# Kernel optimization log

Measured on AMD Instinct MI355X. Metric: run time of the kernel, lower is better.

## Reference

```python
import jax, jax.numpy as jnp
import numpy as np

N = 1_000_000      # number of samples
C = 100            # number of classes
N_BINS = 20        # adaptive-ECE bins (equal-count)
TEMPERATURE = 1.0


def setup_inputs() -> dict:
    key = jax.random.key(0)
    k1, k2 = jax.random.split(key)
    logits = jax.random.normal(k1, (N, C), dtype=jnp.float32)
    labels = jax.random.randint(k2, (N,), 0, C)
    return {"logits": logits, "labels": labels}


def reference(logits, labels):
    # softmax with temperature, top-1 confidence + prediction
    softmaxes = jax.nn.softmax(logits / TEMPERATURE, axis=1)
    confidences = jnp.max(softmaxes, axis=1)            # [N]
    predictions = jnp.argmax(softmaxes, axis=1)         # [N]
    accuracies = (predictions == labels).astype(confidences.dtype)  # [N]

    # sort by confidence ascending; carry accuracies along
    order = jnp.argsort(confidences)
    conf_sorted = confidences[order]
    acc_sorted = accuracies[order]

    num = logits.shape[0]
    window = num // N_BINS            # samples per adaptive bin
    n_full = num // window            # number of flushed bins (== N_BINS when divisible)
    m = n_full * window

    # equal-count binning == reshape + mean (replaces the per-sample python loop)
    conf_bins = conf_sorted[:m].reshape(n_full, window).mean(axis=1)  # avg conf / bin
    acc_bins = acc_sorted[:m].reshape(n_full, window).mean(axis=1)    # accuracy / bin

    ece = jnp.sum(jnp.abs(conf_bins - acc_bins)) * (window / num)
    return jnp.reshape(ece, (1,)), acc_bins
```

## Files before the change

### kernel.cpp

```cpp
#include <hip/hip_runtime.h>
#include <stdint.h>

typedef uint32_t u32;
typedef uint64_t u64;
typedef uint8_t  u8;

#define KEY_MIN   0x3C000000u
#define SUBSHIFT  10
#define NBUCK     57344
#define NBINS     20
#define NB        19

__device__ __forceinline__ u32 bucket_of(u32 key) {
    if (key < KEY_MIN) return 0u;
    u32 b = (key - KEY_MIN) >> SUBSHIFT;
    return b < (u32)NBUCK ? b : (u32)(NBUCK - 1);
}

__global__ __launch_bounds__(256) void k1_conf100(
        const float* __restrict__ logits, const int* __restrict__ labels,
        u32* __restrict__ keys, u8* __restrict__ accb, u32* __restrict__ hist,
        int N) {
    const int C4 = 25;
    int lane = threadIdx.x & 63;
    int wid  = (blockIdx.x * (blockDim.x >> 6)) + (threadIdx.x >> 6);
    int g    = lane >> 4;
    int sub  = lane & 15;
    int r    = wid * 4 + g;
    if (r >= N) return;

    const float4* row4 = (const float4*)(logits + (size_t)r * 100);
    float4 v0 = row4[sub];
    float4 v1;
    bool has2 = (sub + 16) < C4;
    if (has2) v1 = row4[sub + 16];
    else      v1 = make_float4(-3.4e38f, -3.4e38f, -3.4e38f, -3.4e38f);

    float m = v0.x; int am = 4 * sub;
    if (v0.y > m) { m = v0.y; am = 4 * sub + 1; }
    if (v0.z > m) { m = v0.z; am = 4 * sub + 2; }
    if (v0.w > m) { m = v0.w; am = 4 * sub + 3; }
    int b2 = 64 + 4 * sub;
    if (v1.x > m) { m = v1.x; am = b2; }
    if (v1.y > m) { m = v1.y; am = b2 + 1; }
    if (v1.z > m) { m = v1.z; am = b2 + 2; }
    if (v1.w > m) { m = v1.w; am = b2 + 3; }

    #pragma unroll
    for (int off = 8; off >= 1; off >>= 1) {
        float om = __shfl_xor(m, off);
        int   oa = __shfl_xor(am, off);
        if (om > m || (om == m && oa < am)) { m = om; am = oa; }
    }

    float s = __expf(v0.x - m) + __expf(v0.y - m) + __expf(v0.z - m) + __expf(v0.w - m);
    if (has2) s += __expf(v1.x - m) + __expf(v1.y - m) + __expf(v1.z - m) + __expf(v1.w - m);
    #pragma unroll
    for (int off = 8; off >= 1; off >>= 1) s += __shfl_xor(s, off);

    if (sub == 0) {
        float conf = 1.0f / s;
        u32 key = __float_as_uint(conf);
        keys[r] = key;
        accb[r] = (labels[r] == am) ? (u8)1 : (u8)0;
        atomicAdd(&hist[bucket_of(key)], 1u);
    }
}

__global__ __launch_bounds__(256) void k1_generic(
        const float* __restrict__ logits, const int* __restrict__ labels,
        u32* __restrict__ keys, u8* __restrict__ accb, u32* __restrict__ hist,
        int N, int C) {
    int i = blockIdx.x * blockDim.x + threadIdx.x;
    if (i >= N) return;
    const float* row = logits + (size_t)i * (size_t)C;
    float m = -3.4e38f, s = 0.f;
    int am = 0;
    for (int c = 0; c < C; c++) {
        float v = row[c];
        float nm = fmaxf(m, v); am = (v > m) ? c : am;
        s = s * __expf(m - nm) + __expf(v - nm); m = nm;
    }
    float conf = 1.0f / s;
    u32 key = __float_as_uint(conf);
    keys[i] = key;
    accb[i] = (labels[i] == am) ? (u8)1 : (u8)0;
    atomicAdd(&hist[bucket_of(key)], 1u);
}

__global__ void k2_scan(const u32* __restrict__ hist, u32* __restrict__ meta,
                        u32 W) {
    __shared__ u32 sp[1024];
    int t = threadIdx.x;
    const int PER = NBUCK / 1024;
    u32 s = 0;
    for (int k = 0; k < PER; k++) s += hist[t * PER + k];
    sp[t] = s; __syncthreads();
    for (int d = 1; d < 1024; d <<= 1) {
        u32 v = (t >= d) ? sp[t - d] : 0u;
        __syncthreads();
        sp[t] += v;
        __syncthreads();
    }
    u32 cum = sp[t] - s;
    for (int k = 0; k < PER; k++) {
        u32 c = hist[t * PER + k];
        if (c) {
            for (int j = 0; j < NB; j++) {
                u32 r = (u32)(j + 1) * W;
                if (cum < r && r <= cum + c) {
                    meta[j] = (u32)(t * PER + k);
                    meta[NB + j] = r - cum;
                }
            }
        }
        cum += c;
    }
}

__global__ __launch_bounds__(256) void k3_subhist(
        const u32* __restrict__ keys, const u32* __restrict__ meta,
        u32* __restrict__ subhist, int N) {
    __shared__ u32 sB[NB];
    if (threadIdx.x < NB) sB[threadIdx.x] = meta[threadIdx.x];
    __syncthreads();
    int total4 = N >> 2;
    const uint4* k4 = (const uint4*)keys;
    for (int i = blockIdx.x * blockDim.x + threadIdx.x; i < total4;
         i += gridDim.x * blockDim.x) {
        uint4 kv = k4[i];
        u32 ks[4] = {kv.x, kv.y, kv.z, kv.w};
        #pragma unroll
        for (int e = 0; e < 4; e++) {
            u32 b = bucket_of(ks[e]);
            #pragma unroll
            for (int j = 0; j < NB; j++)
                if (b == sB[j]) atomicAdd(&subhist[j * 1024 + (ks[e] & 1023u)], 1u);
        }
    }
    for (int i = (total4 << 2) + blockIdx.x * blockDim.x + threadIdx.x; i < N;
         i += gridDim.x * blockDim.x) {
        u32 k = keys[i];
        u32 b = bucket_of(k);
        for (int j = 0; j < NB; j++)
            if (b == sB[j]) atomicAdd(&subhist[j * 1024 + (k & 1023u)], 1u);
    }
}

__global__ void k4_resolve(const u32* __restrict__ subhist, u32* __restrict__ meta) {
    int j = blockIdx.x;
    int t = threadIdx.x;
    __shared__ u32 sh[256];
    u32 v[4];
    #pragma unroll
    for (int k = 0; k < 4; k++) v[k] = subhist[j * 1024 + t * 4 + k];
    u32 tsum = v[0] + v[1] + v[2] + v[3];
    sh[t] = tsum; __syncthreads();
    for (int d = 1; d < 256; d <<= 1) {
        u32 x = (t >= d) ? sh[t - d] : 0u;
        __syncthreads(); sh[t] += x; __syncthreads();
    }
    u32 run = sh[t] - tsum;
    u32 off = meta[NB + j];
    u32 bkt = meta[j];
    #pragma unroll
    for (int k = 0; k < 4; k++) {
        if (run < off && off <= run + v[k])
            meta[2 * NB + j] = KEY_MIN + (bkt << SUBSHIFT) + (u32)(t * 4 + k);
        run += v[k];
    }
}

__global__ __launch_bounds__(256) void k7_accum(
        const u32* __restrict__ keys, const u8* __restrict__ accb,
        const u32* __restrict__ meta, u64* __restrict__ confQ,
        u32* __restrict__ accCnt, int N) {
    __shared__ unsigned long long lc[4][NBINS];
    __shared__ u32 la[4][NBINS];
    __shared__ u32 sK[NB];
    int t = threadIdx.x;
    int w = t >> 6;
    if (t < 4 * NBINS) { lc[t / NBINS][t % NBINS] = 0ull; la[t / NBINS][t % NBINS] = 0u; }
    if (t < NB) sK[t] = meta[2 * NB + t];
    __syncthreads();
    int total4 = N >> 2;
    const uint4*  k4 = (const uint4*)keys;
    const uchar4* a4 = (const uchar4*)accb;
    for (int i = blockIdx.x * blockDim.x + t; i < total4; i += gridDim.x * blockDim.x) {
        uint4  kv = k4[i];
        uchar4 av = a4[i];
        u32 ks[4] = {kv.x, kv.y, kv.z, kv.w};
        u32 as[4] = {av.x, av.y, av.z, av.w};
        #pragma unroll
        for (int e = 0; e < 4; e++) {
            int bin = 0;
            #pragma unroll
            for (int j = 0; j < NB; j++) bin += (ks[e] > sK[j]) ? 1 : 0;
            float conf = __uint_as_float(ks[e]);
            u64 q = (u64)(conf * 4294967296.0f);
            atomicAdd(&lc[w][bin], (unsigned long long)q);
            atomicAdd(&la[w][bin], as[e]);
        }
    }
    for (int i = (total4 << 2) + blockIdx.x * blockDim.x + t; i < N;
         i += gridDim.x * blockDim.x) {
        u32 k = keys[i];
        int bin = 0;
        for (int j = 0; j < NB; j++) bin += (k > sK[j]) ? 1 : 0;
        u64 q = (u64)(__uint_as_float(k) * 4294967296.0f);
        atomicAdd(&lc[w][bin], (unsigned long long)q);
        atomicAdd(&la[w][bin], (u32)accb[i]);
    }
    __syncthreads();
    if (t < NBINS) {
        unsigned long long cq = lc[0][t] + lc[1][t] + lc[2][t] + lc[3][t];
        u32 ac = la[0][t] + la[1][t] + la[2][t] + la[3][t];
        if (cq) atomicAdd((unsigned long long*)&confQ[t], cq);
        if (ac) atomicAdd(&accCnt[t], ac);
    }
}

__global__ void k8_final(const u64* __restrict__ confQ, const u32* __restrict__ accCnt,
                         float* __restrict__ out, int W, int N) {
    if (threadIdx.x == 0 && blockIdx.x == 0) {
        double ece = 0.0;
        for (int b = 0; b < NBINS; b++) {
            double cm = (double)confQ[b] * (1.0 / 4294967296.0) / (double)W;
            double am = (double)accCnt[b] / (double)W;
            ece += fabs(cm - am);
            out[1 + b] = (float)am;
        }
        out[0] = (float)(ece * (double)W / (double)N);
    }
}

extern "C" void kernel_launch(void* const* d_in, const int* in_sizes, int n_in,
                              void* d_out, int out_size, void* d_ws, size_t ws_size,
                              hipStream_t stream) {
    const float* logits = (const float*)d_in[0];
    const int*   labels = (const int*)d_in[1];
    int N = in_sizes[1];
    int C = in_sizes[0] / N;
    float* out = (float*)d_out;

    u8* ws = (u8*)d_ws;
    u32* keys = (u32*)ws;
    u8*  accb = ws + (size_t)4 * N;
    size_t aux = ((size_t)5 * N + 255) & ~(size_t)255;
    u64* confQ   = (u64*)(ws + aux);
    u32* accCnt  = (u32*)(ws + aux + 160);
    u32* hist    = (u32*)(ws + aux + 256);
    u32* subhist = (u32*)(ws + aux + 229632);
    u32* meta    = (u32*)(ws + aux + 307456);
    size_t zbytes = 307456 + 228;

    hipMemsetAsync(ws + aux, 0, zbytes, stream);

    u32 W = (u32)(N / NBINS);

    if (C == 100) {
        int blocks1 = (N + 15) / 16;
        k1_conf100<<<blocks1, 256, 0, stream>>>(logits, labels, keys, accb, hist, N);
    } else {
        int blocks1 = (N + 255) / 256;
        k1_generic<<<blocks1, 256, 0, stream>>>(logits, labels, keys, accb, hist, N, C);
    }
    k2_scan   <<<1, 1024, 0, stream>>>(hist, meta, W);
    k3_subhist<<<1024, 256, 0, stream>>>(keys, meta, subhist, N);
    k4_resolve<<<NB, 256, 0, stream>>>(subhist, meta);
    k7_accum  <<<1024, 256, 0, stream>>>(keys, accb, meta, confQ, accCnt, N);
    k8_final  <<<1, 64, 0, stream>>>(confQ, accCnt, out, (int)W, N);
}
```

Baseline: 190.5 us.

## Grid-stride softmax with prefetch, coarser histogram, fuse final ECE into accum kernel

The first kernel becomes persistent with a fixed block count, and each 16-lane group prefetches the next row's logits while it reduces the current row. The coarse histogram shrinks to 14336 buckets with 4096-wide sub-ranges, so the scan kernel can stage the whole histogram in LDS, and the resolve kernel reads it with vector loads. The final ECE computation is folded into the accumulation kernel through a last-block-done atomic counter, which removes one launch. The coarser buckets may make the refinement pass collide more on atomics, and the persistent grid lowers the number of waves in flight.

```diff
diff --git a/kernel.cpp b/kernel.cpp
--- a/kernel.cpp
+++ b/kernel.cpp
@@ -6,10 +6,12 @@
 typedef uint8_t  u8;
 
 #define KEY_MIN   0x3C000000u
-#define SUBSHIFT  10
-#define NBUCK     57344
+#define SUBSHIFT  12
+#define NBUCK     14336
+#define SUBRANGE  4096
 #define NBINS     20
 #define NB        19
+#define K1BLK     2048
 
 __device__ __forceinline__ u32 bucket_of(u32 key) {
     if (key < KEY_MIN) return 0u;
@@ -21,49 +23,57 @@
         const float* __restrict__ logits, const int* __restrict__ labels,
         u32* __restrict__ keys, u8* __restrict__ accb, u32* __restrict__ hist,
         int N) {
-    const int C4 = 25;
     int lane = threadIdx.x & 63;
     int wid  = (blockIdx.x * (blockDim.x >> 6)) + (threadIdx.x >> 6);
     int g    = lane >> 4;
     int sub  = lane & 15;
-    int r    = wid * 4 + g;
+    int gid  = wid * 4 + g;
+    int G    = (gridDim.x * blockDim.x) >> 4;
+    bool has2 = sub < 9;
+    const float4 NEG = make_float4(-3.4e38f, -3.4e38f, -3.4e38f, -3.4e38f);
+
+    int r = gid;
     if (r >= N) return;
-
-    const float4* row4 = (const float4*)(logits + (size_t)r * 100);
-    float4 v0 = row4[sub];
-    float4 v1;
-    bool has2 = (sub + 16) < C4;
-    if (has2) v1 = row4[sub + 16];
-    else      v1 = make_float4(-3.4e38f, -3.4e38f, -3.4e38f, -3.4e38f);
-
-    float m = v0.x; int am = 4 * sub;
-    if (v0.y > m) { m = v0.y; am = 4 * sub + 1; }
-    if (v0.z > m) { m = v0.z; am = 4 * sub + 2; }
-    if (v0.w > m) { m = v0.w; am = 4 * sub + 3; }
-    int b2 = 64 + 4 * sub;
-    if (v1.x > m) { m = v1.x; am = b2; }
-    if (v1.y > m) { m = v1.y; am = b2 + 1; }
-    if (v1.z > m) { m = v1.z; am = b2 + 2; }
-    if (v1.w > m) { m = v1.w; am = b2 + 3; }
-
-    #pragma unroll
-    for (int off = 8; off >= 1; off >>= 1) {
-        float om = __shfl_xor(m, off);
-        int   oa = __shfl_xor(am, off);
-        if (om > m || (om == m && oa < am)) { m = om; am = oa; }
-    }
-
-    float s = __expf(v0.x - m) + __expf(v0.y - m) + __expf(v0.z - m) + __expf(v0.w - m);
-    if (has2) s += __expf(v1.x - m) + __expf(v1.y - m) + __expf(v1.z - m) + __expf(v1.w - m);
-    #pragma unroll
-    for (int off = 8; off >= 1; off >>= 1) s += __shfl_xor(s, off);
-
-    if (sub == 0) {
-        float conf = 1.0f / s;
-        u32 key = __float_as_uint(conf);
-        keys[r] = key;
-        accb[r] = (labels[r] == am) ? (u8)1 : (u8)0;
-        atomicAdd(&hist[bucket_of(key)], 1u);
+    const float4* rp = (const float4*)(logits + (size_t)r * 100);
+    float4 a0 = rp[sub];
+    float4 a1 = has2 ? rp[sub + 16] : NEG;
+
+    while (true) {
+        int rn = r + G;
+        bool more = rn < N;
+        const float4* rq = (const float4*)(logits + (size_t)(more ? rn : 0) * 100);
+        float4 b0 = rq[sub];
+        float4 b1 = has2 ? rq[sub + 16] : NEG;
+
+        float m = a0.x; int am = 4 * sub;
+        if (a0.y > m) { m = a0.y; am = 4 * sub + 1; }
+        if (a0.z > m) { m = a0.z; am = 4 * sub + 2; }
+        if (a0.w > m) { m = a0.w; am = 4 * sub + 3; }
+        int c2 = 64 + 4 * sub;
+        if (a1.x > m) { m = a1.x; am = c2; }
+        if (a1.y > m) { m = a1.y; am = c2 + 1; }
+        if (a1.z > m) { m = a1.z; am = c2 + 2; }
+        if (a1.w > m) { m = a1.w; am = c2 + 3; }
+        #pragma unroll
+        for (int off = 8; off >= 1; off >>= 1) {
+            float om = __shfl_xor(m, off);
+            int   oa = __shfl_xor(am, off);
+            if (om > m || (om == m && oa < am)) { m = om; am = oa; }
+        }
+        float s = __expf(a0.x - m) + __expf(a0.y - m) + __expf(a0.z - m) + __expf(a0.w - m);
+        if (has2) s += __expf(a1.x - m) + __expf(a1.y - m) + __expf(a1.z - m) + __expf(a1.w - m);
+        #pragma unroll
+        for (int off = 8; off >= 1; off >>= 1) s += __shfl_xor(s, off);
+
+        if (sub == 0) {
+            float conf = 1.0f / s;
+            u32 key = __float_as_uint(conf);
+            keys[r] = key;
+            accb[r] = (labels[r] == am) ? (u8)1 : (u8)0;
+            atomicAdd(&hist[bucket_of(key)], 1u);
+        }
+        if (!more) break;
+        r = rn; a0 = b0; a1 = b1;
     }
 }
 
@@ -71,40 +81,44 @@
         const float* __restrict__ logits, const int* __restrict__ labels,
         u32* __restrict__ keys, u8* __restrict__ accb, u32* __restrict__ hist,
         int N, int C) {
-    int i = blockIdx.x * blockDim.x + threadIdx.x;
-    if (i >= N) return;
-    const float* row = logits + (size_t)i * (size_t)C;
-    float m = -3.4e38f, s = 0.f;
-    int am = 0;
-    for (int c = 0; c < C; c++) {
-        float v = row[c];
-        float nm = fmaxf(m, v); am = (v > m) ? c : am;
-        s = s * __expf(m - nm) + __expf(v - nm); m = nm;
-    }
-    float conf = 1.0f / s;
-    u32 key = __float_as_uint(conf);
-    keys[i] = key;
-    accb[i] = (labels[i] == am) ? (u8)1 : (u8)0;
-    atomicAdd(&hist[bucket_of(key)], 1u);
-}
-
-__global__ void k2_scan(const u32* __restrict__ hist, u32* __restrict__ meta,
-                        u32 W) {
+    for (int i = blockIdx.x * blockDim.x + threadIdx.x; i < N;
+         i += gridDim.x * blockDim.x) {
+        const float* row = logits + (size_t)i * (size_t)C;
+        float m = -3.4e38f, s = 0.f;
+        int am = 0;
+        for (int c = 0; c < C; c++) {
+            float v = row[c];
+            float nm = fmaxf(m, v); am = (v > m) ? c : am;
+            s = s * __expf(m - nm) + __expf(v - nm); m = nm;
+        }
+        float conf = 1.0f / s;
+        u32 key = __float_as_uint(conf);
+        keys[i] = key;
+        accb[i] = (labels[i] == am) ? (u8)1 : (u8)0;
+        atomicAdd(&hist[bucket_of(key)], 1u);
+    }
+}
+
+__global__ __launch_bounds__(1024) void k2_scan(
+        const u32* __restrict__ hist, u32* __restrict__ meta, u32 W) {
+    __shared__ u32 lh[NBUCK];
     __shared__ u32 sp[1024];
     int t = threadIdx.x;
+    #pragma unroll
+    for (int k = 0; k < NBUCK / 1024; k++) lh[k * 1024 + t] = hist[k * 1024 + t];
+    __syncthreads();
     const int PER = NBUCK / 1024;
     u32 s = 0;
-    for (int k = 0; k < PER; k++) s += hist[t * PER + k];
+    #pragma unroll
+    for (int k = 0; k < PER; k++) s += lh[t * PER + k];
     sp[t] = s; __syncthreads();
     for (int d = 1; d < 1024; d <<= 1) {
         u32 v = (t >= d) ? sp[t - d] : 0u;
-        __syncthreads();
-        sp[t] += v;
-        __syncthreads();
+        __syncthreads(); sp[t] += v; __syncthreads();
     }
     u32 cum = sp[t] - s;
     for (int k = 0; k < PER; k++) {
-        u32 c = hist[t * PER + k];
+        u32 c = lh[t * PER + k];
         if (c) {
             for (int j = 0; j < NB; j++) {
                 u32 r = (u32)(j + 1) * W;
@@ -135,7 +149,8 @@
             u32 b = bucket_of(ks[e]);
             #pragma unroll
             for (int j = 0; j < NB; j++)
-                if (b == sB[j]) atomicAdd(&subhist[j * 1024 + (ks[e] & 1023u)], 1u);
+                if (b == sB[j])
+                    atomicAdd(&subhist[j * SUBRANGE + (ks[e] & (SUBRANGE - 1))], 1u);
         }
     }
     for (int i = (total4 << 2) + blockIdx.x * blockDim.x + threadIdx.x; i < N;
@@ -143,18 +158,23 @@
         u32 k = keys[i];
         u32 b = bucket_of(k);
         for (int j = 0; j < NB; j++)
-            if (b == sB[j]) atomicAdd(&subhist[j * 1024 + (k & 1023u)], 1u);
-    }
-}
-
-__global__ void k4_resolve(const u32* __restrict__ subhist, u32* __restrict__ meta) {
+            if (b == sB[j])
+                atomicAdd(&subhist[j * SUBRANGE + (k & (SUBRANGE - 1))], 1u);
+    }
+}
+
+__global__ __launch_bounds__(256) void k4_resolve(
+        const u32* __restrict__ subhist, u32* __restrict__ meta) {
     int j = blockIdx.x;
     int t = threadIdx.x;
     __shared__ u32 sh[256];
-    u32 v[4];
-    #pragma unroll
-    for (int k = 0; k < 4; k++) v[k] = subhist[j * 1024 + t * 4 + k];
-    u32 tsum = v[0] + v[1] + v[2] + v[3];
+    const uint4* s4 = (const uint4*)(subhist + j * SUBRANGE);
+    uint4 v[4];
+    #pragma unroll
+    for (int q = 0; q < 4; q++) v[q] = s4[t * 4 + q];
+    u32 tsum = 0;
+    #pragma unroll
+    for (int q = 0; q < 4; q++) tsum += v[q].x + v[q].y + v[q].z + v[q].w;
     sh[t] = tsum; __syncthreads();
     for (int d = 1; d < 256; d <<= 1) {
         u32 x = (t >= d) ? sh[t - d] : 0u;
@@ -164,23 +184,30 @@
     u32 off = meta[NB + j];
     u32 bkt = meta[j];
     #pragma unroll
-    for (int k = 0; k < 4; k++) {
-        if (run < off && off <= run + v[k])
-            meta[2 * NB + j] = KEY_MIN + (bkt << SUBSHIFT) + (u32)(t * 4 + k);
-        run += v[k];
+    for (int q = 0; q < 4; q++) {
+        u32 e[4] = {v[q].x, v[q].y, v[q].z, v[q].w};
+        #pragma unroll
+        for (int c = 0; c < 4; c++) {
+            if (run < off && off <= run + e[c])
+                meta[2 * NB + j] = KEY_MIN + (bkt << SUBSHIFT) + (u32)(t * 16 + q * 4 + c);
+            run += e[c];
+        }
     }
 }
 
 __global__ __launch_bounds__(256) void k7_accum(
         const u32* __restrict__ keys, const u8* __restrict__ accb,
         const u32* __restrict__ meta, u64* __restrict__ confQ,
-        u32* __restrict__ accCnt, int N) {
+        u32* __restrict__ accCnt, u32* __restrict__ done,
+        float* __restrict__ out, int N, u32 W) {
     __shared__ unsigned long long lc[4][NBINS];
     __shared__ u32 la[4][NBINS];
     __shared__ u32 sK[NB];
+    __shared__ u32 isLast;
     int t = threadIdx.x;
     int w = t >> 6;
     if (t < 4 * NBINS) { lc[t / NBINS][t % NBINS] = 0ull; la[t / NBINS][t % NBINS] = 0u; }
+    if (t == 0) isLast = 0u;
     if (t < NB) sK[t] = meta[2 * NB + t];
     __syncthreads();
     int total4 = N >> 2;
@@ -196,8 +223,7 @@
             int bin = 0;
             #pragma unroll
             for (int j = 0; j < NB; j++) bin += (ks[e] > sK[j]) ? 1 : 0;
-            float conf = __uint_as_float(ks[e]);
-            u64 q = (u64)(conf * 4294967296.0f);
+            u64 q = (u64)(__uint_as_float(ks[e]) * 4294967296.0f);
             atomicAdd(&lc[w][bin], (unsigned long long)q);
             atomicAdd(&la[w][bin], as[e]);
         }
@@ -218,15 +244,20 @@
         if (cq) atomicAdd((unsigned long long*)&confQ[t], cq);
         if (ac) atomicAdd(&accCnt[t], ac);
     }
-}
-
-__global__ void k8_final(const u64* __restrict__ confQ, const u32* __restrict__ accCnt,
-                         float* __restrict__ out, int W, int N) {
-    if (threadIdx.x == 0 && blockIdx.x == 0) {
+    __syncthreads();
+    if (t == 0) {
+        __threadfence();
+        u32 old = __hip_atomic_fetch_add(done, 1u, __ATOMIC_ACQ_REL, __HIP_MEMORY_SCOPE_AGENT);
+        if (old == gridDim.x - 1) isLast = 1u;
+    }
+    __syncthreads();
+    if (isLast && t == 0) {
         double ece = 0.0;
         for (int b = 0; b < NBINS; b++) {
-            double cm = (double)confQ[b] * (1.0 / 4294967296.0) / (double)W;
-            double am = (double)accCnt[b] / (double)W;
+            u64 cq = __hip_atomic_load(&confQ[b], __ATOMIC_RELAXED, __HIP_MEMORY_SCOPE_AGENT);
+            u32 ac = __hip_atomic_load(&accCnt[b], __ATOMIC_RELAXED, __HIP_MEMORY_SCOPE_AGENT);
+            double cm = (double)cq * (1.0 / 4294967296.0) / (double)W;
+            double am = (double)ac / (double)W;
             ece += fabs(cm - am);
             out[1 + b] = (float)am;
         }
@@ -249,25 +280,23 @@
     size_t aux = ((size_t)5 * N + 255) & ~(size_t)255;
     u64* confQ   = (u64*)(ws + aux);
     u32* accCnt  = (u32*)(ws + aux + 160);
+    u32* done    = (u32*)(ws + aux + 240);
     u32* hist    = (u32*)(ws + aux + 256);
-    u32* subhist = (u32*)(ws + aux + 229632);
-    u32* meta    = (u32*)(ws + aux + 307456);
-    size_t zbytes = 307456 + 228;
+    u32* subhist = (u32*)(ws + aux + 57600);
+    u32* meta    = (u32*)(ws + aux + 368896);
+    size_t zbytes = 368896 + 228;
 
     hipMemsetAsync(ws + aux, 0, zbytes, stream);
 
     u32 W = (u32)(N / NBINS);
 
     if (C == 100) {
-        int blocks1 = (N + 15) / 16;
-        k1_conf100<<<blocks1, 256, 0, stream>>>(logits, labels, keys, accb, hist, N);
+        k1_conf100<<<K1BLK, 256, 0, stream>>>(logits, labels, keys, accb, hist, N);
     } else {
-        int blocks1 = (N + 255) / 256;
-        k1_generic<<<blocks1, 256, 0, stream>>>(logits, labels, keys, accb, hist, N, C);
+        k1_generic<<<K1BLK, 256, 0, stream>>>(logits, labels, keys, accb, hist, N, C);
     }
     k2_scan   <<<1, 1024, 0, stream>>>(hist, meta, W);
     k3_subhist<<<1024, 256, 0, stream>>>(keys, meta, subhist, N);
     k4_resolve<<<NB, 256, 0, stream>>>(subhist, meta);
-    k7_accum  <<<1024, 256, 0, stream>>>(keys, accb, meta, confQ, accCnt, N);
-    k8_final  <<<1, 64, 0, stream>>>(confQ, accCnt, out, (int)W, N);
-}
+    k7_accum  <<<1024, 256, 0, stream>>>(keys, accb, meta, confQ, accCnt, done, out, N, W);
+}
```

Result: slower. 273.3 us (+43.5%).
